# Performance work log

Hardware: AMD Instinct MI355X
Metric: run time of the kernel (lower is better)

The kernel has to match this reference:

```python
import jax, jax.numpy as jnp
import numpy as np

N_USER = 60000
N_ITEM = 40000
N = N_USER + N_ITEM          # total nodes
D = 64                        # embed_size
E_HALF = 400000               # undirected interactions; E = 2*E_HALF symmetric directed edges
N_LAYERS = 3                  # len(args.layer_size)
BETA = 0.5                    # self.beta_
EPS = 1e-8                    # torch cosine_similarity eps


def setup_inputs() -> dict:
    key = jax.random.key(0)
    ks = jax.random.split(key, 8)
    # symmetric bipartite edge list: (u, n_user+i) and its reverse
    u = jax.random.randint(ks[0], (E_HALF,), 0, N_USER)
    it = jax.random.randint(ks[1], (E_HALF,), 0, N_ITEM) + N_USER
    src = jnp.concatenate([u, it])
    dst = jnp.concatenate([it, u])
    # rev_perm[e] gives the index of edge (dst[e], src[e])
    rev_perm = jnp.concatenate([jnp.arange(E_HALF) + E_HALF, jnp.arange(E_HALF)])
    vals_half = jax.random.uniform(ks[2], (E_HALF,), minval=0.01, maxval=0.1)
    adj_vals = jnp.concatenate([vals_half, vals_half])  # symmetric normalized adjacency values
    user_emb = 0.1 * jax.random.normal(ks[3], (N_USER, D), dtype=jnp.float32)
    item_emb = 0.1 * jax.random.normal(ks[4], (N_ITEM, D), dtype=jnp.float32)
    W_prune = jax.random.normal(ks[5], (1, 2), dtype=jnp.float32) / jnp.sqrt(2.0)
    b_prune = jnp.zeros((1,), dtype=jnp.float32)
    users = jax.random.randint(ks[6], (2048,), 0, N_USER)
    items = jax.random.randint(ks[7], (2048,), 0, N_ITEM)
    return {"users": users, "items": items, "user_emb": user_emb, "item_emb": item_emb,
            "W_prune": W_prune, "b_prune": b_prune, "src": src, "dst": dst,
            "rev_perm": rev_perm, "adj_vals": adj_vals}


def _computer(user_emb, item_emb, W_prune, b_prune, adj_vals, src, dst, rev_perm):
    emb = jnp.concatenate([user_emb, item_emb], axis=0)  # [N, D]
    embs = [emb]
    mem = adj_vals                                        # memory = adj values at start
    for _ in range(N_LAYERS):
        es, ed = emb[src], emb[dst]                       # [E, D] edge gathers
        # per-edge cosine similarity (torch eps clamp on denominator)
        num = jnp.sum(es * ed, axis=-1)
        den = jnp.maximum(jnp.linalg.norm(es, axis=-1) * jnp.linalg.norm(ed, axis=-1), EPS)
        cos = num / den
        # row-wise L1 normalization over adjacency nonzeros (sklearn normalize, norm='l1')
        rowsum = jax.ops.segment_sum(jnp.abs(cos), src, num_segments=N)
        denom = rowsum[src]
        coef = cos / jnp.where(denom > 0, denom, 1.0)
        # pruning: Linear(2,1) on [coef[r,c], coef[c,r]], sigmoid, keep iff > 0.5
        cv = jnp.stack([coef, coef[rev_perm]], axis=-1)   # [E, 2]
        p = jax.nn.sigmoid(cv @ W_prune.T + b_prune)[:, 0]
        decision = (p > 0.5).astype(coef.dtype)
        coef = coef * decision
        # memory EMA, then elementwise multiply with adjacency -> propagation weights
        mem = BETA * mem + (1.0 - BETA) * coef
        g = mem * adj_vals
        # sparse matmul: out[r] = sum_c A[r,c] * emb[c]
        emb = jax.ops.segment_sum(g[:, None] * ed, src, num_segments=N)
        embs.append(emb)
    light_out = jnp.mean(jnp.stack(embs, axis=1), axis=1)  # [N, D]
    return light_out[:N_USER], light_out[N_USER:]


def reference(users, items, user_emb, item_emb, W_prune, b_prune, src, dst, rev_perm, adj_vals):
    all_users, all_items = _computer(user_emb, item_emb, W_prune, b_prune, adj_vals, src, dst, rev_perm)
    users_emb = all_users[users]                          # [Bu, D]
    items_emb = all_items[items]                          # [Bi, D]
    return jax.nn.sigmoid(users_emb @ items_emb.T)        # [Bu, Bi]
```

## Files before the change

kernel.cpp:

```cpp
#include <hip/hip_runtime.h>
#include <math.h>


#define DD 64
typedef unsigned int u32;

__device__ __forceinline__ float bflo(u32 u) { return __uint_as_float(u << 16); }
__device__ __forceinline__ float bfhi(u32 u) { return __uint_as_float(u & 0xFFFF0000u); }
__device__ __forceinline__ u32 bfpk(float lo, float hi) {
    u32 a = __float_as_uint(lo), b = __float_as_uint(hi);
    a = (a + 0x7FFFu + ((a >> 16) & 1u)) >> 16;
    b = (b + 0x7FFFu + ((b >> 16) & 1u)) & 0xFFFF0000u;
    return a | b;
}
__device__ __forceinline__ void unp16(uint4 q0, uint4 q1, float* f) {
    f[0]=bflo(q0.x); f[1]=bfhi(q0.x); f[2]=bflo(q0.y); f[3]=bfhi(q0.y);
    f[4]=bflo(q0.z); f[5]=bfhi(q0.z); f[6]=bflo(q0.w); f[7]=bfhi(q0.w);
    f[8]=bflo(q1.x); f[9]=bfhi(q1.x); f[10]=bflo(q1.y); f[11]=bfhi(q1.y);
    f[12]=bflo(q1.z); f[13]=bfhi(q1.z); f[14]=bflo(q1.w); f[15]=bfhi(q1.w);
}


__global__ __launch_bounds__(256) void hist_k(const int* __restrict__ src,
                                              int* __restrict__ deg,
                                              int* __restrict__ rank, int E) {
    int e = blockIdx.x * blockDim.x + threadIdx.x;
    if (e < E) rank[e] = atomicAdd(&deg[src[e]], 1);
}

__global__ __launch_bounds__(256) void scan1_k(const int* __restrict__ in,
                                               int* __restrict__ out,
                                               int* __restrict__ partial, int M) {
    __shared__ int sh[256];
    int base = blockIdx.x * 1024;
    int t = threadIdx.x;
    int i0 = base + t * 4;
    int v0 = (i0 + 0 < M) ? in[i0 + 0] : 0;
    int v1 = (i0 + 1 < M) ? in[i0 + 1] : 0;
    int v2 = (i0 + 2 < M) ? in[i0 + 2] : 0;
    int v3 = (i0 + 3 < M) ? in[i0 + 3] : 0;
    int tsum = v0 + v1 + v2 + v3;
    sh[t] = tsum;
    __syncthreads();
    for (int off = 1; off < 256; off <<= 1) {
        int x = (t >= off) ? sh[t - off] : 0;
        __syncthreads();
        sh[t] += x;
        __syncthreads();
    }
    int texcl = sh[t] - tsum;
    if (i0 + 0 < M) out[i0 + 0] = texcl;
    if (i0 + 1 < M) out[i0 + 1] = texcl + v0;
    if (i0 + 2 < M) out[i0 + 2] = texcl + v0 + v1;
    if (i0 + 3 < M) out[i0 + 3] = texcl + v0 + v1 + v2;
    if (t == 255) partial[blockIdx.x] = sh[255];
}

__global__ __launch_bounds__(256) void scan2_k(int* __restrict__ partial, int nc) {
    __shared__ int sh[256];
    int t = threadIdx.x;
    int v = (t < nc) ? partial[t] : 0;
    sh[t] = v;
    __syncthreads();
    for (int off = 1; off < 256; off <<= 1) {
        int x = (t >= off) ? sh[t - off] : 0;
        __syncthreads();
        sh[t] += x;
        __syncthreads();
    }
    if (t < nc) partial[t] = sh[t] - v;
}

__global__ __launch_bounds__(256) void scan3_k(int* __restrict__ out,
                                               const int* __restrict__ partial, int M) {
    int i = blockIdx.x * blockDim.x + threadIdx.x;
    if (i < M) out[i] += partial[i >> 10];
}

__global__ __launch_bounds__(256) void scatter_k(const int* __restrict__ src,
                                                 const int* __restrict__ dst,
                                                 const float* __restrict__ adj,
                                                 const int* __restrict__ rp,
                                                 const int* __restrict__ rank,
                                                 int4* __restrict__ ent, int EH) {
    int e = blockIdx.x * blockDim.x + threadIdx.x;
    if (e >= EH) return;
    int u = src[e], i = dst[e];
    int ab = __float_as_int(adj[e]);
    int posU = rp[u] + rank[e];
    int posI = rp[i] + rank[e + EH];
    ent[posU] = make_int4(i, ab, posU, 0);
    ent[posI] = make_int4(u, ab, posU, 0);
}


__global__ __launch_bounds__(256) void cvt_k(const float* __restrict__ ue,
                                             const float* __restrict__ ie,
                                             u32* __restrict__ tab, int NU, int Nn) {
    int idx = blockIdx.x * blockDim.x + threadIdx.x;
    if (idx >= Nn * 32) return;
    int node = idx >> 5, po = idx & 31;
    const float2* srow = (node < NU) ? (const float2*)(ue + (size_t)node * DD)
                                     : (const float2*)(ie + (size_t)(node - NU) * DD);
    float2 f = srow[po];
    tab[idx] = bfpk(f.x, f.y);
}


__global__ __launch_bounds__(256) void node_norms_k(const u32* __restrict__ tab,
                                                    float* __restrict__ norms, int n) {
    int quad = (blockIdx.x * blockDim.x + threadIdx.x) >> 2;
    int l4   = threadIdx.x & 3;
    if (quad >= n) return;
    const uint4* p = (const uint4*)(tab + (size_t)quad * 32 + l4 * 8);
    float f[16];
    unp16(p[0], p[1], f);
    float s = 0.f;
#pragma unroll
    for (int i = 0; i < 16; ++i) s += f[i] * f[i];
    s += __shfl_xor(s, 1, 64);
    s += __shfl_xor(s, 2, 64);
    if (l4 == 0) norms[quad] = sqrtf(s);
}

__global__ __launch_bounds__(256) void cos_row_k(const u32* __restrict__ tab,
                                                 const float* __restrict__ norms,
                                                 const int* __restrict__ rp,
                                                 const int4* __restrict__ ent,
                                                 float* __restrict__ cosc,
                                                 float* __restrict__ rowsum, int NU) {
    int quad = (blockIdx.x * blockDim.x + threadIdx.x) >> 2;
    int l4   = threadIdx.x & 3;
    if (quad >= NU) return;
    int r  = quad;
    int p0 = rp[r], p1 = rp[r + 1];
    const uint4* ap = (const uint4*)(tab + (size_t)r * 32 + l4 * 8);
    float A[16];
    unp16(ap[0], ap[1], A);
    float nr = norms[r];
    float rs = 0.f;
    for (int p = p0; p < p1; ++p) {
        int d = ent[p].x;
        const uint4* bp_ = (const uint4*)(tab + (size_t)d * 32 + l4 * 8);
        float B[16];
        unp16(bp_[0], bp_[1], B);
        float dot = 0.f;
#pragma unroll
        for (int i = 0; i < 16; ++i) dot += A[i] * B[i];
        dot += __shfl_xor(dot, 1, 64);
        dot += __shfl_xor(dot, 2, 64);
        float c = dot / fmaxf(nr * norms[d], 1e-8f);
        if (l4 == 0) {
            cosc[p] = c;
            atomicAdd(&rowsum[d], fabsf(c));
        }
        rs += fabsf(c);
    }
    if (l4 == 0) rowsum[r] = rs;
}

__global__ __launch_bounds__(256) void spmm_fused_k(const u32* __restrict__ tab,
                                                    const int* __restrict__ rp,
                                                    const int4* __restrict__ ent,
                                                    const float* __restrict__ cosc,
                                                    const float* __restrict__ rowsum,
                                                    const float* __restrict__ Wp,
                                                    const float* __restrict__ bp,
                                                    float* __restrict__ memc, int useAdj,
                                                    u32* __restrict__ outtab, int N) {
    int quad = (blockIdx.x * blockDim.x + threadIdx.x) >> 2;
    int l4   = threadIdx.x & 3;
    if (quad >= N) return;
    int r  = quad;
    int p0 = rp[r], p1 = rp[r + 1];
    float w0 = Wp[0], w1 = Wp[1], bb = bp[0];
    float rs  = rowsum[r];
    float rsg = rs > 0.f ? rs : 1.f;
    float a16[16];
#pragma unroll
    for (int i = 0; i < 16; ++i) a16[i] = 0.f;
    for (int p = p0; p < p1; ++p) {
        int4 t = ent[p];
        int d = t.x;
        float a  = __int_as_float(t.y);
        float cv = cosc[t.z];
        float rd  = rowsum[d];
        float rdg = rd > 0.f ? rd : 1.f;
        float c  = cv / rsg;
        float cr = cv / rdg;
        float z  = w0 * c + w1 * cr + bb;
        float kept = (z > 0.f) ? c : 0.f;
        float mprev = useAdj ? a : memc[p];
        float m = 0.5f * mprev + 0.5f * kept;
        if (l4 == 0) memc[p] = m;
        float g = m * a;
        const uint4* bp_ = (const uint4*)(tab + (size_t)d * 32 + l4 * 8);
        float B[16];
        unp16(bp_[0], bp_[1], B);
#pragma unroll
        for (int i = 0; i < 16; ++i) a16[i] += g * B[i];
    }
    uint4 o0, o1;
    o0.x = bfpk(a16[0], a16[1]);  o0.y = bfpk(a16[2], a16[3]);
    o0.z = bfpk(a16[4], a16[5]);  o0.w = bfpk(a16[6], a16[7]);
    o1.x = bfpk(a16[8], a16[9]);  o1.y = bfpk(a16[10], a16[11]);
    o1.z = bfpk(a16[12], a16[13]); o1.w = bfpk(a16[14], a16[15]);
    uint4* op = (uint4*)(outtab + (size_t)r * 32 + l4 * 8);
    op[0] = o0;
    op[1] = o1;
}

__global__ __launch_bounds__(256) void sel_spmm_k(const u32* __restrict__ tab,
                                                  const int* __restrict__ rp,
                                                  const int4* __restrict__ ent,
                                                  const float* __restrict__ cosc,
                                                  const float* __restrict__ rowsum,
                                                  const float* __restrict__ Wp,
                                                  const float* __restrict__ bp,
                                                  const float* __restrict__ memc,
                                                  const int* __restrict__ users,
                                                  const int* __restrict__ items,
                                                  float* __restrict__ acc,
                                                  int BU, int BI, int NU) {
    int quad = (blockIdx.x * blockDim.x + threadIdx.x) >> 2;
    int l4   = threadIdx.x & 3;
    if (quad >= BU + BI) return;
    int r  = (quad < BU) ? users[quad] : (NU + items[quad - BU]);
    int p0 = rp[r], p1 = rp[r + 1];
    float w0 = Wp[0], w1 = Wp[1], bb = bp[0];
    float rs  = rowsum[r];
    float rsg = rs > 0.f ? rs : 1.f;
    float a16[16];
#pragma unroll
    for (int i = 0; i < 16; ++i) a16[i] = 0.f;
    for (int p = p0; p < p1; ++p) {
        int4 t = ent[p];
        int d = t.x;
        float a  = __int_as_float(t.y);
        float cv = cosc[t.z];
        float rd  = rowsum[d];
        float rdg = rd > 0.f ? rd : 1.f;
        float c  = cv / rsg;
        float cr = cv / rdg;
        float z  = w0 * c + w1 * cr + bb;
        float kept = (z > 0.f) ? c : 0.f;
        float m = 0.5f * memc[p] + 0.5f * kept;
        float g = m * a;
        const uint4* bp_ = (const uint4*)(tab + (size_t)d * 32 + l4 * 8);
        float B[16];
        unp16(bp_[0], bp_[1], B);
#pragma unroll
        for (int i = 0; i < 16; ++i) a16[i] += g * B[i];
    }
    float4* av = (float4*)acc;
#pragma unroll
    for (int k = 0; k < 4; ++k) {
        float4 o = av[(size_t)quad * 16 + l4 * 4 + k];
        o.x += a16[k * 4 + 0]; o.y += a16[k * 4 + 1];
        o.z += a16[k * 4 + 2]; o.w += a16[k * 4 + 3];
        av[(size_t)quad * 16 + l4 * 4 + k] = o;
    }
}


__global__ __launch_bounds__(256) void acc_init_k(const float* __restrict__ ue,
                                                  const float* __restrict__ ie,
                                                  const int* __restrict__ users,
                                                  const int* __restrict__ items,
                                                  float* __restrict__ acc,
                                                  int BU, int BI, int NU) {
    int quad = (blockIdx.x * blockDim.x + threadIdx.x) >> 2;
    int l4   = threadIdx.x & 3;
    if (quad >= BU + BI) return;
    int node = (quad < BU) ? users[quad] : (NU + items[quad - BU]);
    const float4* srow = (node < NU) ? (const float4*)(ue + (size_t)node * DD)
                                     : (const float4*)(ie + (size_t)(node - NU) * DD);
    float4* av = (float4*)acc;
#pragma unroll
    for (int k = 0; k < 4; ++k)
        av[(size_t)quad * 16 + l4 * 4 + k] = srow[l4 * 4 + k];
}

__global__ __launch_bounds__(256) void acc_upd_k(const u32* __restrict__ tab,
                                                 const int* __restrict__ users,
                                                 const int* __restrict__ items,
                                                 float* __restrict__ acc,
                                                 int BU, int BI, int NU) {
    int quad = (blockIdx.x * blockDim.x + threadIdx.x) >> 2;
    int l4   = threadIdx.x & 3;
    if (quad >= BU + BI) return;
    int node = (quad < BU) ? users[quad] : (NU + items[quad - BU]);
    const uint4* p = (const uint4*)(tab + (size_t)node * 32 + l4 * 8);
    float f[16];
    unp16(p[0], p[1], f);
    float4* av = (float4*)acc;
#pragma unroll
    for (int k = 0; k < 4; ++k) {
        float4 o = av[(size_t)quad * 16 + l4 * 4 + k];
        o.x += f[k * 4 + 0]; o.y += f[k * 4 + 1];
        o.z += f[k * 4 + 2]; o.w += f[k * 4 + 3];
        av[(size_t)quad * 16 + l4 * 4 + k] = o;
    }
}

__global__ __launch_bounds__(256) void final_gemm_k(const float* __restrict__ acc,
                                                    float* __restrict__ out,
                                                    int BU, int BI) {
    __shared__ float Us[64][65];
    __shared__ float Is[64][65];
    int t = threadIdx.x;
    int i0 = blockIdx.y * 64, j0 = blockIdx.x * 64;
#pragma unroll
    for (int i = 0; i < 4; ++i) {
        int f4 = t + i * 256;
        int r = f4 >> 4, c4 = (f4 & 15) * 4;
        float4 u4 = *(const float4*)&acc[(size_t)(i0 + r) * DD + c4];
        float4 v4 = *(const float4*)&acc[(size_t)(BU + j0 + r) * DD + c4];
        Us[r][c4 + 0] = u4.x; Us[r][c4 + 1] = u4.y;
        Us[r][c4 + 2] = u4.z; Us[r][c4 + 3] = u4.w;
        Is[r][c4 + 0] = v4.x; Is[r][c4 + 1] = v4.y;
        Is[r][c4 + 2] = v4.z; Is[r][c4 + 3] = v4.w;
    }
    __syncthreads();
    int tx = t & 15, ty = t >> 4;
    float s[4][4];
#pragma unroll
    for (int i = 0; i < 4; ++i)
#pragma unroll
        for (int j = 0; j < 4; ++j) s[i][j] = 0.f;
    for (int k = 0; k < 64; ++k) {
        float u[4], v[4];
#pragma unroll
        for (int i = 0; i < 4; ++i) u[i] = Us[ty * 4 + i][k];
#pragma unroll
        for (int j = 0; j < 4; ++j) v[j] = Is[tx * 4 + j][k];
#pragma unroll
        for (int i = 0; i < 4; ++i)
#pragma unroll
            for (int j = 0; j < 4; ++j) s[i][j] += u[i] * v[j];
    }
#pragma unroll
    for (int i = 0; i < 4; ++i) {
        float4 o;
        o.x = 1.f / (1.f + expf(-s[i][0] * 0.0625f));
        o.y = 1.f / (1.f + expf(-s[i][1] * 0.0625f));
        o.z = 1.f / (1.f + expf(-s[i][2] * 0.0625f));
        o.w = 1.f / (1.f + expf(-s[i][3] * 0.0625f));
        *(float4*)&out[(size_t)(i0 + ty * 4 + i) * BI + j0 + tx * 4] = o;
    }
}


extern "C" void kernel_launch(void* const* d_in, const int* in_sizes, int n_in,
                              void* d_out, int out_size, void* d_ws, size_t ws_size,
                              hipStream_t stream) {
    const int*   users    = (const int*)d_in[0];
    const int*   items    = (const int*)d_in[1];
    const float* user_emb = (const float*)d_in[2];
    const float* item_emb = (const float*)d_in[3];
    const float* Wp       = (const float*)d_in[4];
    const float* bp       = (const float*)d_in[5];
    const int*   src      = (const int*)d_in[6];
    const int*   dst      = (const int*)d_in[7];
    const float* adj      = (const float*)d_in[9];

    int BU = in_sizes[0];
    int BI = in_sizes[1];
    int NU = in_sizes[2] / DD;
    int NI = in_sizes[3] / DD;
    int Nn = NU + NI;
    int E  = in_sizes[6];
    int EH = E / 2;
    int M  = Nn + 1;
    int Mp = (M + 3) & ~3;

    int4*  ent    = (int4*)d_ws;
    u32*   tabA   = (u32*)(ent + E);
    u32*   tabB   = tabA + (size_t)Nn * 32;
    float* norms  = (float*)(tabB + (size_t)Nn * 32);
    float* rowsum = norms + Nn;
    float* cosc   = rowsum + Nn;
    float* memc   = cosc + EH;
    float* acc    = memc + E;
    int*   deg    = (int*)(acc + (size_t)(BU + BI) * DD);
    int*   rp     = deg + Mp;
    int*   rank   = rp + Mp;
    int*   partial= rank + E;

    int eb  = (E + 255) / 256;
    int ehb = (EH + 255) / 256;
    int nc  = (M + 1023) / 1024;

    hipMemsetAsync(deg, 0, sizeof(int) * (size_t)M, stream);
    hist_k<<<eb, 256, 0, stream>>>(src, deg, rank, E);
    scan1_k<<<nc, 256, 0, stream>>>(deg, rp, partial, M);
    scan2_k<<<1, 256, 0, stream>>>(partial, nc);
    scan3_k<<<(M + 255) / 256, 256, 0, stream>>>(rp, partial, M);
    scatter_k<<<ehb, 256, 0, stream>>>(src, dst, adj, rp, rank, ent, EH);

    cvt_k<<<(Nn * 32 + 255) / 256, 256, 0, stream>>>(user_emb, item_emb, tabA, NU, Nn);
    int selBlocks = (4 * (BU + BI) + 255) / 256;
    acc_init_k<<<selBlocks, 256, 0, stream>>>(user_emb, item_emb, users, items, acc,
                                              BU, BI, NU);

    int rowBlocksU = (4 * NU + 255) / 256;
    int rowBlocksN = (4 * Nn + 255) / 256;
    u32* cur = tabA;
    u32* nxt = tabB;
    for (int layer = 0; layer < 3; ++layer) {
        hipMemsetAsync(rowsum + NU, 0, sizeof(float) * (size_t)NI, stream);
        node_norms_k<<<rowBlocksN, 256, 0, stream>>>(cur, norms, Nn);
        cos_row_k<<<rowBlocksU, 256, 0, stream>>>(cur, norms, rp, ent, cosc, rowsum, NU);
        if (layer < 2) {
            spmm_fused_k<<<rowBlocksN, 256, 0, stream>>>(cur, rp, ent, cosc, rowsum,
                                                         Wp, bp, memc, layer == 0 ? 1 : 0,
                                                         nxt, Nn);
            acc_upd_k<<<selBlocks, 256, 0, stream>>>(nxt, users, items, acc, BU, BI, NU);
            u32* t = cur; cur = nxt; nxt = t;
        } else {
            sel_spmm_k<<<selBlocks, 256, 0, stream>>>(cur, rp, ent, cosc, rowsum,
                                                      Wp, bp, memc, users, items,
                                                      acc, BU, BI, NU);
        }
    }

    dim3 grid(BI / 64, BU / 64);
    final_gemm_k<<<grid, 256, 0, stream>>>(acc, (float*)d_out, BU, BI);
}
```

Measured before the change: 398.4 us.

## Compact edge entries to int2 with side cosine index; unroll gather loops by four

Shrinks each CSR entry from int4 to int2 (neighbor, adj). For item rows it adds a separate cidx array that maps each position back to its user-side cosine slot, while user rows index cosc directly. The cosine, SpMM and selected-SpMM loops are also unrolled by four, so several row gathers are in flight at once to hide memory latency. In exchange, item rows pay an extra indirect load and register pressure goes up.

Measured after the change: 358.7 us. 10.0% less time.

```diff
diff --git a/kernel.cpp b/kernel.cpp
--- a/kernel.cpp
+++ b/kernel.cpp
@@ -82,15 +82,17 @@
                                                  const float* __restrict__ adj,
                                                  const int* __restrict__ rp,
                                                  const int* __restrict__ rank,
-                                                 int4* __restrict__ ent, int EH) {
+                                                 int2* __restrict__ ent,
+                                                 int* __restrict__ cidx, int EH) {
     int e = blockIdx.x * blockDim.x + threadIdx.x;
     if (e >= EH) return;
     int u = src[e], i = dst[e];
     int ab = __float_as_int(adj[e]);
     int posU = rp[u] + rank[e];
     int posI = rp[i] + rank[e + EH];
-    ent[posU] = make_int4(i, ab, posU, 0);
-    ent[posI] = make_int4(u, ab, posU, 0);
+    ent[posU] = make_int2(i, ab);
+    ent[posI] = make_int2(u, ab);
+    cidx[posI - EH] = posU;
 }
 
 
@@ -126,7 +128,7 @@
 __global__ __launch_bounds__(256) void cos_row_k(const u32* __restrict__ tab,
                                                  const float* __restrict__ norms,
                                                  const int* __restrict__ rp,
-                                                 const int4* __restrict__ ent,
+                                                 const int2* __restrict__ ent,
                                                  float* __restrict__ cosc,
                                                  float* __restrict__ rowsum, int NU) {
     int quad = (blockIdx.x * blockDim.x + threadIdx.x) >> 2;
@@ -139,11 +141,54 @@
     unp16(ap[0], ap[1], A);
     float nr = norms[r];
     float rs = 0.f;
-    for (int p = p0; p < p1; ++p) {
+    int p = p0;
+    for (; p + 4 <= p1; p += 4) {
+        int d0 = ent[p].x, d1 = ent[p+1].x, d2 = ent[p+2].x, d3 = ent[p+3].x;
+        const uint4* q0 = (const uint4*)(tab + (size_t)d0 * 32 + l4 * 8);
+        const uint4* q1 = (const uint4*)(tab + (size_t)d1 * 32 + l4 * 8);
+        const uint4* q2 = (const uint4*)(tab + (size_t)d2 * 32 + l4 * 8);
+        const uint4* q3 = (const uint4*)(tab + (size_t)d3 * 32 + l4 * 8);
+        uint4 b00 = q0[0], b01 = q0[1];
+        uint4 b10 = q1[0], b11 = q1[1];
+        uint4 b20 = q2[0], b21 = q2[1];
+        uint4 b30 = q3[0], b31 = q3[1];
+        float n0 = norms[d0], n1 = norms[d1], n2 = norms[d2], n3 = norms[d3];
+        float B[16];
+        float dt0 = 0.f, dt1 = 0.f, dt2 = 0.f, dt3 = 0.f;
+        unp16(b00, b01, B);
+#pragma unroll
+        for (int i = 0; i < 16; ++i) dt0 += A[i] * B[i];
+        unp16(b10, b11, B);
+#pragma unroll
+        for (int i = 0; i < 16; ++i) dt1 += A[i] * B[i];
+        unp16(b20, b21, B);
+#pragma unroll
+        for (int i = 0; i < 16; ++i) dt2 += A[i] * B[i];
+        unp16(b30, b31, B);
+#pragma unroll
+        for (int i = 0; i < 16; ++i) dt3 += A[i] * B[i];
+        dt0 += __shfl_xor(dt0, 1, 64); dt0 += __shfl_xor(dt0, 2, 64);
+        dt1 += __shfl_xor(dt1, 1, 64); dt1 += __shfl_xor(dt1, 2, 64);
+        dt2 += __shfl_xor(dt2, 1, 64); dt2 += __shfl_xor(dt2, 2, 64);
+        dt3 += __shfl_xor(dt3, 1, 64); dt3 += __shfl_xor(dt3, 2, 64);
+        float c0 = dt0 / fmaxf(nr * n0, 1e-8f);
+        float c1 = dt1 / fmaxf(nr * n1, 1e-8f);
+        float c2 = dt2 / fmaxf(nr * n2, 1e-8f);
+        float c3 = dt3 / fmaxf(nr * n3, 1e-8f);
+        if (l4 == 0) {
+            cosc[p]   = c0; atomicAdd(&rowsum[d0], fabsf(c0));
+            cosc[p+1] = c1; atomicAdd(&rowsum[d1], fabsf(c1));
+            cosc[p+2] = c2; atomicAdd(&rowsum[d2], fabsf(c2));
+            cosc[p+3] = c3; atomicAdd(&rowsum[d3], fabsf(c3));
+        }
+        rs += fabsf(c0) + fabsf(c1) + fabsf(c2) + fabsf(c3);
+    }
+    for (; p < p1; ++p) {
         int d = ent[p].x;
-        const uint4* bp_ = (const uint4*)(tab + (size_t)d * 32 + l4 * 8);
+        const uint4* q = (const uint4*)(tab + (size_t)d * 32 + l4 * 8);
+        uint4 b0 = q[0], b1 = q[1];
         float B[16];
-        unp16(bp_[0], bp_[1], B);
+        unp16(b0, b1, B);
         float dot = 0.f;
 #pragma unroll
         for (int i = 0; i < 16; ++i) dot += A[i] * B[i];
@@ -161,49 +206,86 @@
 
 __global__ __launch_bounds__(256) void spmm_fused_k(const u32* __restrict__ tab,
                                                     const int* __restrict__ rp,
-                                                    const int4* __restrict__ ent,
+                                                    const int2* __restrict__ ent,
+                                                    const int* __restrict__ cidx,
                                                     const float* __restrict__ cosc,
                                                     const float* __restrict__ rowsum,
                                                     const float* __restrict__ Wp,
                                                     const float* __restrict__ bp,
                                                     float* __restrict__ memc, int useAdj,
-                                                    u32* __restrict__ outtab, int N) {
+                                                    u32* __restrict__ outtab,
+                                                    int NU, int EH, int N) {
     int quad = (blockIdx.x * blockDim.x + threadIdx.x) >> 2;
     int l4   = threadIdx.x & 3;
     if (quad >= N) return;
     int r  = quad;
     int p0 = rp[r], p1 = rp[r + 1];
+    bool isU = (r < NU);
     float w0 = Wp[0], w1 = Wp[1], bb = bp[0];
     float rs  = rowsum[r];
     float rsg = rs > 0.f ? rs : 1.f;
     float a16[16];
 #pragma unroll
     for (int i = 0; i < 16; ++i) a16[i] = 0.f;
-    for (int p = p0; p < p1; ++p) {
-        int4 t = ent[p];
-        int d = t.x;
-        float a  = __int_as_float(t.y);
-        float cv = cosc[t.z];
-        float rd  = rowsum[d];
-        float rdg = rd > 0.f ? rd : 1.f;
-        float c  = cv / rsg;
-        float cr = cv / rdg;
-        float z  = w0 * c + w1 * cr + bb;
-        float kept = (z > 0.f) ? c : 0.f;
-        float mprev = useAdj ? a : memc[p];
-        float m = 0.5f * mprev + 0.5f * kept;
-        if (l4 == 0) memc[p] = m;
-        float g = m * a;
-        const uint4* bp_ = (const uint4*)(tab + (size_t)d * 32 + l4 * 8);
+    int p = p0;
+    for (; p + 4 <= p1; p += 4) {
+        int2 t0 = ent[p], t1 = ent[p+1], t2 = ent[p+2], t3 = ent[p+3];
+        int c0i = isU ? p   : cidx[p   - EH];
+        int c1i = isU ? p+1 : cidx[p+1 - EH];
+        int c2i = isU ? p+2 : cidx[p+2 - EH];
+        int c3i = isU ? p+3 : cidx[p+3 - EH];
+        const uint4* q0 = (const uint4*)(tab + (size_t)t0.x * 32 + l4 * 8);
+        const uint4* q1 = (const uint4*)(tab + (size_t)t1.x * 32 + l4 * 8);
+        const uint4* q2 = (const uint4*)(tab + (size_t)t2.x * 32 + l4 * 8);
+        const uint4* q3 = (const uint4*)(tab + (size_t)t3.x * 32 + l4 * 8);
+        uint4 b00 = q0[0], b01 = q0[1];
+        uint4 b10 = q1[0], b11 = q1[1];
+        uint4 b20 = q2[0], b21 = q2[1];
+        uint4 b30 = q3[0], b31 = q3[1];
+        float cv0 = cosc[c0i], cv1 = cosc[c1i], cv2 = cosc[c2i], cv3 = cosc[c3i];
+        float rd0 = rowsum[t0.x], rd1 = rowsum[t1.x];
+        float rd2 = rowsum[t2.x], rd3 = rowsum[t3.x];
+        float mp0 = useAdj ? __int_as_float(t0.y) : memc[p];
+        float mp1 = useAdj ? __int_as_float(t1.y) : memc[p+1];
+        float mp2 = useAdj ? __int_as_float(t2.y) : memc[p+2];
+        float mp3 = useAdj ? __int_as_float(t3.y) : memc[p+3];
         float B[16];
-        unp16(bp_[0], bp_[1], B);
-#pragma unroll
-        for (int i = 0; i < 16; ++i) a16[i] += g * B[i];
-    }
+#define EDGE(cv, rd, mp, ty, bA, bB, pp)                                    \
+        {                                                                   \
+            float a = __int_as_float(ty);                                   \
+            float rdg = rd > 0.f ? rd : 1.f;                                \
+            float c  = cv / rsg;                                            \
+            float cr = cv / rdg;                                            \
+            float z  = w0 * c + w1 * cr + bb;                               \
+            float kept = (z > 0.f) ? c : 0.f;                               \
+            float m = 0.5f * mp + 0.5f * kept;                              \
+            if (l4 == 0) memc[pp] = m;                                      \
+            float g = m * a;                                                \
+            unp16(bA, bB, B);                                               \
+            _Pragma("unroll")                                               \
+            for (int i = 0; i < 16; ++i) a16[i] += g * B[i];                \
+        }
+        EDGE(cv0, rd0, mp0, t0.y, b00, b01, p)
+        EDGE(cv1, rd1, mp1, t1.y, b10, b11, p+1)
+        EDGE(cv2, rd2, mp2, t2.y, b20, b21, p+2)
+        EDGE(cv3, rd3, mp3, t3.y, b30, b31, p+3)
+    }
+    for (; p < p1; ++p) {
+        int2 t = ent[p];
+        int ci = isU ? p : cidx[p - EH];
+        const uint4* q = (const uint4*)(tab + (size_t)t.x * 32 + l4 * 8);
+        uint4 b0 = q[0], b1 = q[1];
+        float cv = cosc[ci];
+        float rd = rowsum[t.x];
+        float mp = useAdj ? __int_as_float(t.y) : memc[p];
+        float B[16];
+        EDGE(cv, rd, mp, t.y, b0, b1, p)
+    }
+#undef EDGE
     uint4 o0, o1;
-    o0.x = bfpk(a16[0], a16[1]);  o0.y = bfpk(a16[2], a16[3]);
-    o0.z = bfpk(a16[4], a16[5]);  o0.w = bfpk(a16[6], a16[7]);
-    o1.x = bfpk(a16[8], a16[9]);  o1.y = bfpk(a16[10], a16[11]);
+    o0.x = bfpk(a16[0], a16[1]);   o0.y = bfpk(a16[2], a16[3]);
+    o0.z = bfpk(a16[4], a16[5]);   o0.w = bfpk(a16[6], a16[7]);
+    o1.x = bfpk(a16[8], a16[9]);   o1.y = bfpk(a16[10], a16[11]);
     o1.z = bfpk(a16[12], a16[13]); o1.w = bfpk(a16[14], a16[15]);
     uint4* op = (uint4*)(outtab + (size_t)r * 32 + l4 * 8);
     op[0] = o0;
@@ -212,7 +294,8 @@
 
 __global__ __launch_bounds__(256) void sel_spmm_k(const u32* __restrict__ tab,
                                                   const int* __restrict__ rp,
-                                                  const int4* __restrict__ ent,
+                                                  const int2* __restrict__ ent,
+                                                  const int* __restrict__ cidx,
                                                   const float* __restrict__ cosc,
                                                   const float* __restrict__ rowsum,
                                                   const float* __restrict__ Wp,
@@ -221,37 +304,70 @@
                                                   const int* __restrict__ users,
                                                   const int* __restrict__ items,
                                                   float* __restrict__ acc,
-                                                  int BU, int BI, int NU) {
+                                                  int BU, int BI, int NU, int EH) {
     int quad = (blockIdx.x * blockDim.x + threadIdx.x) >> 2;
     int l4   = threadIdx.x & 3;
     if (quad >= BU + BI) return;
     int r  = (quad < BU) ? users[quad] : (NU + items[quad - BU]);
     int p0 = rp[r], p1 = rp[r + 1];
+    bool isU = (r < NU);
     float w0 = Wp[0], w1 = Wp[1], bb = bp[0];
     float rs  = rowsum[r];
     float rsg = rs > 0.f ? rs : 1.f;
     float a16[16];
 #pragma unroll
     for (int i = 0; i < 16; ++i) a16[i] = 0.f;
-    for (int p = p0; p < p1; ++p) {
-        int4 t = ent[p];
-        int d = t.x;
-        float a  = __int_as_float(t.y);
-        float cv = cosc[t.z];
-        float rd  = rowsum[d];
-        float rdg = rd > 0.f ? rd : 1.f;
-        float c  = cv / rsg;
-        float cr = cv / rdg;
-        float z  = w0 * c + w1 * cr + bb;
-        float kept = (z > 0.f) ? c : 0.f;
-        float m = 0.5f * memc[p] + 0.5f * kept;
-        float g = m * a;
-        const uint4* bp_ = (const uint4*)(tab + (size_t)d * 32 + l4 * 8);
+    int p = p0;
+    for (; p + 4 <= p1; p += 4) {
+        int2 t0 = ent[p], t1 = ent[p+1], t2 = ent[p+2], t3 = ent[p+3];
+        int c0i = isU ? p   : cidx[p   - EH];
+        int c1i = isU ? p+1 : cidx[p+1 - EH];
+        int c2i = isU ? p+2 : cidx[p+2 - EH];
+        int c3i = isU ? p+3 : cidx[p+3 - EH];
+        const uint4* q0 = (const uint4*)(tab + (size_t)t0.x * 32 + l4 * 8);
+        const uint4* q1 = (const uint4*)(tab + (size_t)t1.x * 32 + l4 * 8);
+        const uint4* q2 = (const uint4*)(tab + (size_t)t2.x * 32 + l4 * 8);
+        const uint4* q3 = (const uint4*)(tab + (size_t)t3.x * 32 + l4 * 8);
+        uint4 b00 = q0[0], b01 = q0[1];
+        uint4 b10 = q1[0], b11 = q1[1];
+        uint4 b20 = q2[0], b21 = q2[1];
+        uint4 b30 = q3[0], b31 = q3[1];
+        float cv0 = cosc[c0i], cv1 = cosc[c1i], cv2 = cosc[c2i], cv3 = cosc[c3i];
+        float rd0 = rowsum[t0.x], rd1 = rowsum[t1.x];
+        float rd2 = rowsum[t2.x], rd3 = rowsum[t3.x];
+        float mm0 = memc[p], mm1 = memc[p+1], mm2 = memc[p+2], mm3 = memc[p+3];
         float B[16];
-        unp16(bp_[0], bp_[1], B);
-#pragma unroll
-        for (int i = 0; i < 16; ++i) a16[i] += g * B[i];
-    }
+#define EDGES(cv, rd, mm, ty, bA, bB)                                       \
+        {                                                                   \
+            float a = __int_as_float(ty);                                   \
+            float rdg = rd > 0.f ? rd : 1.f;                                \
+            float c  = cv / rsg;                                            \
+            float cr = cv / rdg;                                            \
+            float z  = w0 * c + w1 * cr + bb;                               \
+            float kept = (z > 0.f) ? c : 0.f;                               \
+            float m = 0.5f * mm + 0.5f * kept;                              \
+            float g = m * a;                                                \
+            unp16(bA, bB, B);                                               \
+            _Pragma("unroll")                                               \
+            for (int i = 0; i < 16; ++i) a16[i] += g * B[i];                \
+        }
+        EDGES(cv0, rd0, mm0, t0.y, b00, b01)
+        EDGES(cv1, rd1, mm1, t1.y, b10, b11)
+        EDGES(cv2, rd2, mm2, t2.y, b20, b21)
+        EDGES(cv3, rd3, mm3, t3.y, b30, b31)
+    }
+    for (; p < p1; ++p) {
+        int2 t = ent[p];
+        int ci = isU ? p : cidx[p - EH];
+        const uint4* q = (const uint4*)(tab + (size_t)t.x * 32 + l4 * 8);
+        uint4 b0 = q[0], b1 = q[1];
+        float cv = cosc[ci];
+        float rd = rowsum[t.x];
+        float mm = memc[p];
+        float B[16];
+        EDGES(cv, rd, mm, t.y, b0, b1)
+    }
+#undef EDGES
     float4* av = (float4*)acc;
 #pragma unroll
     for (int k = 0; k < 4; ++k) {
@@ -374,10 +490,11 @@
     int M  = Nn + 1;
     int Mp = (M + 3) & ~3;
 
-    int4*  ent    = (int4*)d_ws;
-    u32*   tabA   = (u32*)(ent + E);
+    u32*   tabA   = (u32*)d_ws;
     u32*   tabB   = tabA + (size_t)Nn * 32;
-    float* norms  = (float*)(tabB + (size_t)Nn * 32);
+    int2*  ent    = (int2*)(tabB + (size_t)Nn * 32);
+    int*   cidx   = (int*)(ent + E);
+    float* norms  = (float*)(cidx + EH);
     float* rowsum = norms + Nn;
     float* cosc   = rowsum + Nn;
     float* memc   = cosc + EH;
@@ -396,7 +513,7 @@
     scan1_k<<<nc, 256, 0, stream>>>(deg, rp, partial, M);
     scan2_k<<<1, 256, 0, stream>>>(partial, nc);
     scan3_k<<<(M + 255) / 256, 256, 0, stream>>>(rp, partial, M);
-    scatter_k<<<ehb, 256, 0, stream>>>(src, dst, adj, rp, rank, ent, EH);
+    scatter_k<<<ehb, 256, 0, stream>>>(src, dst, adj, rp, rank, ent, cidx, EH);
 
     cvt_k<<<(Nn * 32 + 255) / 256, 256, 0, stream>>>(user_emb, item_emb, tabA, NU, Nn);
     int selBlocks = (4 * (BU + BI) + 255) / 256;
@@ -412,15 +529,16 @@
         node_norms_k<<<rowBlocksN, 256, 0, stream>>>(cur, norms, Nn);
         cos_row_k<<<rowBlocksU, 256, 0, stream>>>(cur, norms, rp, ent, cosc, rowsum, NU);
         if (layer < 2) {
-            spmm_fused_k<<<rowBlocksN, 256, 0, stream>>>(cur, rp, ent, cosc, rowsum,
-                                                         Wp, bp, memc, layer == 0 ? 1 : 0,
-                                                         nxt, Nn);
+            spmm_fused_k<<<rowBlocksN, 256, 0, stream>>>(cur, rp, ent, cidx, cosc,
+                                                         rowsum, Wp, bp, memc,
+                                                         layer == 0 ? 1 : 0, nxt,
+                                                         NU, EH, Nn);
             acc_upd_k<<<selBlocks, 256, 0, stream>>>(nxt, users, items, acc, BU, BI, NU);
             u32* t = cur; cur = nxt; nxt = t;
         } else {
-            sel_spmm_k<<<selBlocks, 256, 0, stream>>>(cur, rp, ent, cosc, rowsum,
+            sel_spmm_k<<<selBlocks, 256, 0, stream>>>(cur, rp, ent, cidx, cosc, rowsum,
                                                       Wp, bp, memc, users, items,
-                                                      acc, BU, BI, NU);
+                                                      acc, BU, BI, NU, EH);
         }
     }
 
```
